# Optimization experiments

Measured on AMD Instinct MI355X. Metric: run time of the kernel, lower is better.

## Reference

```python
import jax, jax.numpy as jnp
import numpy as np

EMB_DIM = 1024
D_K = 64
B, S = 4, 4096

def setup_inputs() -> dict:
    key = jax.random.key(0)
    ks = jax.random.split(key, 8)
    inv = 1.0 / np.sqrt(EMB_DIM)
    return {
        "input1": jax.random.normal(ks[0], (B, S, EMB_DIM), dtype=jnp.float32),
        "input2": jax.random.normal(ks[1], (B, S, EMB_DIM), dtype=jnp.float32),
        "Wq": jax.random.uniform(ks[2], (EMB_DIM, D_K), jnp.float32, -inv, inv),
        "bq": jax.random.uniform(ks[3], (D_K,), jnp.float32, -inv, inv),
        "Wk": jax.random.uniform(ks[4], (EMB_DIM, D_K), jnp.float32, -inv, inv),
        "bk": jax.random.uniform(ks[5], (D_K,), jnp.float32, -inv, inv),
        "Wv": jax.random.uniform(ks[6], (EMB_DIM, D_K), jnp.float32, -inv, inv),
        "bv": jax.random.uniform(ks[7], (D_K,), jnp.float32, -inv, inv),
    }

def reference(input1, input2, Wq, bq, Wk, bk, Wv, bv):
    # queries from input2; keys/values from input1 (as in the torch forward)
    q = input2 @ Wq + bq            # [B, Sq, d_k]
    k = input1 @ Wk + bk            # [B, Sk, d_k]
    v = input1 @ Wv + bv            # [B, Sk, d_k]
    scale = 1.0 / jnp.sqrt(jnp.asarray(D_K, q.dtype))
    scores = jnp.einsum("bqd,bkd->bqk", q, k) * scale  # [B, Sq, Sk]
    attn = jax.nn.softmax(scores, axis=-1)
    return jnp.einsum("bqk,bkd->bqd", attn, v)          # [B, Sq, d_k]
```

## Files before the change

### kernel.cpp

```cpp
#include <hip/hip_runtime.h>
#include <hip/hip_bf16.h>

#define E 1024
#define DK 64
#define SEQ 4096
#define NB 4
#define KSCALE 0.18033688011112042f

typedef short bf16x8 __attribute__((ext_vector_type(8)));
typedef short bf16x4 __attribute__((ext_vector_type(4)));
typedef float f32x4 __attribute__((ext_vector_type(4)));

typedef const __attribute__((address_space(1))) unsigned int* gcp;
typedef __attribute__((address_space(3))) unsigned int* lcp;

__device__ inline unsigned short f2bf(float f) {
    unsigned int u = __float_as_uint(f);
    u += 0x7fff + ((u >> 16) & 1);
    return (unsigned short)(u >> 16);
}
__device__ inline unsigned int cvtpk(float a, float b) {
    union { __hip_bfloat162 h; unsigned int u; } x;
    x.h = __float22bfloat162_rn(make_float2(a, b));
    return x.u;
}
__device__ inline bf16x8 cvt8(f32x4 a, f32x4 b) {
    union { unsigned int u[4]; bf16x8 v; } x;
    x.u[0] = cvtpk(a[0], a[1]); x.u[1] = cvtpk(a[2], a[3]);
    x.u[2] = cvtpk(b[0], b[1]); x.u[3] = cvtpk(b[2], b[3]);
    return x.v;
}

__global__ __launch_bounds__(256) void wt_kernel(
    const float* __restrict__ Wq, const float* __restrict__ Wk, const float* __restrict__ Wv,
    unsigned short* __restrict__ wtq, unsigned short* __restrict__ wtk, unsigned short* __restrict__ wtv)
{
    const float* src; unsigned short* dst;
    if (blockIdx.y == 0)      { src = Wq; dst = wtq; }
    else if (blockIdx.y == 1) { src = Wk; dst = wtk; }
    else                      { src = Wv; dst = wtv; }
    const int tid = threadIdx.x;
    const int e0 = blockIdx.x * 64;
    __shared__ float Ws[64][65];
    #pragma unroll
    for (int i = 0; i < 4; ++i) {
        int flat = i * 256 + tid;
        int r = flat >> 4;
        int c4 = (flat & 15) << 2;
        float4 v = *reinterpret_cast<const float4*>(&src[(size_t)(e0 + r) * DK + c4]);
        Ws[c4 + 0][r] = v.x; Ws[c4 + 1][r] = v.y; Ws[c4 + 2][r] = v.z; Ws[c4 + 3][r] = v.w;
    }
    __syncthreads();
    #pragma unroll
    for (int i = 0; i < 4; ++i) {
        int flat = i * 256 + tid;
        int c = flat >> 4;
        int r4 = (flat & 15) << 2;
        ushort4 o;
        o.x = f2bf(Ws[c][r4 + 0]); o.y = f2bf(Ws[c][r4 + 1]);
        o.z = f2bf(Ws[c][r4 + 2]); o.w = f2bf(Ws[c][r4 + 3]);
        *reinterpret_cast<ushort4*>(&dst[(size_t)c * E + e0 + r4]) = o;
    }
}

__global__ __launch_bounds__(256, 4) void proj_kernel(
    const float* __restrict__ in_q, const float* __restrict__ in_kv,
    const unsigned short* __restrict__ wtq, const unsigned short* __restrict__ wtk,
    const unsigned short* __restrict__ wtv,
    const float* __restrict__ bq, const float* __restrict__ bk, const float* __restrict__ bv,
    unsigned short* __restrict__ Qw, unsigned short* __restrict__ Kw, unsigned short* __restrict__ Vtw)
{
    const int tid = threadIdx.x;
    const int w = tid >> 6, lane = tid & 63, quad = lane >> 4, l16 = lane & 15;
    const int row0 = blockIdx.x * 64;
    const bool isQ = (blockIdx.y == 0);
    const float* Arow = (isQ ? in_q : in_kv) + (size_t)(row0 + w * 16 + l16) * E;
    const unsigned short* w0 = isQ ? wtq : wtk;

    __shared__ unsigned short W0s[2][4096];
    __shared__ unsigned short W1s[2][4096];

    const int rl = lane >> 3, pp = lane & 7;

    #pragma unroll
    for (int i = 0; i < 2; ++i) {
        int g = w * 2 + i;
        int r = g * 8 + rl;
        int lc = pp ^ (r & 7);
        __builtin_amdgcn_global_load_lds((gcp)(const void*)(w0 + (size_t)r * E + lc * 8),
                                         (lcp)(void*)&W0s[0][g * 512], 16, 0, 0);
        if (!isQ)
            __builtin_amdgcn_global_load_lds((gcp)(const void*)(wtv + (size_t)r * E + lc * 8),
                                             (lcp)(void*)&W1s[0][g * 512], 16, 0, 0);
    }
    f32x4 a_cur[4];
    #pragma unroll
    for (int ks = 0; ks < 2; ++ks)
        #pragma unroll
        for (int j = 0; j < 2; ++j)
            a_cur[ks * 2 + j] = *reinterpret_cast<const f32x4*>(Arow + ks * 32 + quad * 8 + j * 4);
    __syncthreads();

    f32x4 acc0[4] = {};
    f32x4 acc1[4] = {};

    for (int kb = 0; kb < 16; ++kb) {
        const int cur = kb & 1, nxt = cur ^ 1;
        f32x4 a_nxt[4];
        if (kb < 15) {
            const int ko = (kb + 1) * 64;
            #pragma unroll
            for (int i = 0; i < 2; ++i) {
                int g = w * 2 + i;
                int r = g * 8 + rl;
                int lc = pp ^ (r & 7);
                __builtin_amdgcn_global_load_lds((gcp)(const void*)(w0 + (size_t)r * E + ko + lc * 8),
                                                 (lcp)(void*)&W0s[nxt][g * 512], 16, 0, 0);
                if (!isQ)
                    __builtin_amdgcn_global_load_lds((gcp)(const void*)(wtv + (size_t)r * E + ko + lc * 8),
                                                     (lcp)(void*)&W1s[nxt][g * 512], 16, 0, 0);
            }
            const float* an = Arow + ko;
            #pragma unroll
            for (int ks = 0; ks < 2; ++ks)
                #pragma unroll
                for (int j = 0; j < 2; ++j)
                    a_nxt[ks * 2 + j] = *reinterpret_cast<const f32x4*>(an + ks * 32 + quad * 8 + j * 4);
        }
        #pragma unroll
        for (int ks = 0; ks < 2; ++ks) {
            bf16x8 af = cvt8(a_cur[ks * 2], a_cur[ks * 2 + 1]);
            #pragma unroll
            for (int ct = 0; ct < 4; ++ct) {
                int brow = ct * 16 + l16;
                int pc = (ks * 4 + quad) ^ (brow & 7);
                bf16x8 b0 = *reinterpret_cast<const bf16x8*>(&W0s[cur][brow * 64 + pc * 8]);
                acc0[ct] = __builtin_amdgcn_mfma_f32_16x16x32_bf16(af, b0, acc0[ct], 0, 0, 0);
                if (!isQ) {
                    bf16x8 b1 = *reinterpret_cast<const bf16x8*>(&W1s[cur][brow * 64 + pc * 8]);
                    acc1[ct] = __builtin_amdgcn_mfma_f32_16x16x32_bf16(af, b1, acc1[ct], 0, 0, 0);
                }
            }
        }
        #pragma unroll
        for (int j = 0; j < 4; ++j) a_cur[j] = a_nxt[j];
        if (kb < 15) __syncthreads();
    }

    const int orow0 = row0 + w * 16 + quad * 4;
    #pragma unroll
    for (int ct = 0; ct < 4; ++ct) {
        int col = ct * 16 + l16;
        if (isQ) {
            float bias = bq[col];
            #pragma unroll
            for (int r = 0; r < 4; ++r)
                Qw[(size_t)(orow0 + r) * DK + col] = f2bf(acc0[ct][r] + bias);
        } else {
            float biask = bk[col], biasv = bv[col];
            #pragma unroll
            for (int r = 0; r < 4; ++r) {
                int grow = orow0 + r;
                Kw[(size_t)grow * DK + col] = f2bf((acc0[ct][r] + biask) * KSCALE);
                int bb = grow >> 12;
                int tok = grow & 4095;
                Vtw[((size_t)(bb * 64 + col)) * SEQ + tok] = f2bf(acc1[ct][r] + biasv);
            }
        }
    }
}

__global__ __launch_bounds__(512) void attn_kernel(
    const unsigned short* __restrict__ Qw, const unsigned short* __restrict__ Kw,
    const unsigned short* __restrict__ Vtw, float* __restrict__ Opart, float* __restrict__ Lpart)
{
    const int tid = threadIdx.x;
    const int w = tid >> 6, lane = tid & 63, quad = lane >> 4, l16 = lane & 15;
    const int s = w & 3, h = w >> 2;
    const int kh = blockIdx.x & 1;
    const int b  = (blockIdx.x >> 1) & 3;
    const int qt = blockIdx.x >> 3;

    __shared__ unsigned short Klds[2][8192];
    __shared__ unsigned short Vlds[2][8192];
    __shared__ float LDSf[8][2][16][68];
    __shared__ float LDSl[8][4][16];

    const unsigned short* Ksrc = Kw + ((size_t)b * SEQ + kh * 2048) * DK;
    const unsigned short* Vsrc = Vtw + (size_t)b * 64 * SEQ + kh * 2048;

    const int g0 = w * 2, g1 = w * 2 + 1;
    const int krow0 = g0 * 8 + (lane >> 3), krow1 = g1 * 8 + (lane >> 3);
    const int kcol = ((lane & 7) ^ (lane >> 3)) << 4;
    const int vrow0 = g0 * 4 + (lane >> 4), vrow1 = g1 * 4 + (lane >> 4);
    const int vcol0 = ((lane & 15) ^ (vrow0 & 7)) << 4;
    const int vcol1 = ((lane & 15) ^ (vrow1 & 7)) << 4;

    auto stage = [&](int t, int bb) {
        const char* kb = (const char*)Ksrc + (size_t)t * 16384;
        __builtin_amdgcn_global_load_lds((gcp)(const void*)(kb + krow0 * 128 + kcol),
                                         (lcp)(void*)((char*)Klds[bb] + g0 * 1024), 16, 0, 0);
        __builtin_amdgcn_global_load_lds((gcp)(const void*)(kb + krow1 * 128 + kcol),
                                         (lcp)(void*)((char*)Klds[bb] + g1 * 1024), 16, 0, 0);
        const char* vb = (const char*)Vsrc + t * 256;
        __builtin_amdgcn_global_load_lds((gcp)(const void*)(vb + (size_t)vrow0 * 8192 + vcol0),
                                         (lcp)(void*)((char*)Vlds[bb] + g0 * 1024), 16, 0, 0);
        __builtin_amdgcn_global_load_lds((gcp)(const void*)(vb + (size_t)vrow1 * 8192 + vcol1),
                                         (lcp)(void*)((char*)Vlds[bb] + g1 * 1024), 16, 0, 0);
    };

    stage(0, 0);

    bf16x8 qfb[2][4];
    #pragma unroll
    for (int ks = 0; ks < 2; ++ks)
        #pragma unroll
        for (int ct = 0; ct < 4; ++ct)
            qfb[ks][ct] = *reinterpret_cast<const bf16x8*>(
                &Qw[((size_t)(b * SEQ + qt * 128 + h * 64 + ct * 16 + l16)) * DK + ks * 32 + quad * 8]);

    const int kxor = (l16 & 7) << 4;
    unsigned kf_off[2][2];
    unsigned va_off[2][4];
    #pragma unroll
    for (int t2 = 0; t2 < 2; ++t2) {
        const int kr = s * 32 + t2 * 16 + l16;
        kf_off[t2][0] = (unsigned)(kr * 128 + ((quad * 16) ^ kxor));
        kf_off[t2][1] = (unsigned)(kr * 128 + ((64 + quad * 16) ^ kxor));
        #pragma unroll
        for (int ct = 0; ct < 4; ++ct)
            va_off[t2][ct] = (unsigned)((ct * 16 + l16) * 256 +
                                        ((s * 64 + t2 * 32 + quad * 8) ^ kxor));
    }

    __syncthreads();

    float lp[4] = {0.f, 0.f, 0.f, 0.f};
    f32x4 o[4][4] = {};

    #pragma unroll 1
    for (int i = 0; i < 16; ++i) {
        const int cur = i & 1;
        if (i < 15) stage(i + 1, cur ^ 1);

        #pragma unroll
        for (int t2 = 0; t2 < 2; ++t2) {
            bf16x8 kf0 = *reinterpret_cast<const bf16x8*>((const char*)Klds[cur] + kf_off[t2][0]);
            bf16x8 kf1 = *reinterpret_cast<const bf16x8*>((const char*)Klds[cur] + kf_off[t2][1]);
            bf16x4 va[4];
            #pragma unroll
            for (int ct = 0; ct < 4; ++ct)
                va[ct] = *reinterpret_cast<const bf16x4*>((const char*)Vlds[cur] + va_off[t2][ct]);

            f32x4 sacc[4] = {};
            #pragma unroll
            for (int ct = 0; ct < 4; ++ct) {
                sacc[ct] = __builtin_amdgcn_mfma_f32_16x16x32_bf16(kf0, qfb[0][ct], sacc[ct], 0, 0, 0);
                sacc[ct] = __builtin_amdgcn_mfma_f32_16x16x32_bf16(kf1, qfb[1][ct], sacc[ct], 0, 0, 0);
            }

            #pragma unroll
            for (int cq = 0; cq < 4; ++cq) {
                float p0 = __builtin_amdgcn_exp2f(sacc[cq][0]);
                float p1 = __builtin_amdgcn_exp2f(sacc[cq][1]);
                float p2 = __builtin_amdgcn_exp2f(sacc[cq][2]);
                float p3 = __builtin_amdgcn_exp2f(sacc[cq][3]);
                lp[cq] += (p0 + p1) + (p2 + p3);
                union { unsigned int u[2]; bf16x4 v; } pbu;
                pbu.u[0] = cvtpk(p0, p1);
                pbu.u[1] = cvtpk(p2, p3);
                bf16x4 pb = pbu.v;
                #pragma unroll
                for (int cd = 0; cd < 4; ++cd)
                    o[cd][cq] = __builtin_amdgcn_mfma_f32_16x16x16bf16_1k(va[cd], pb, o[cd][cq], 0, 0, 0);
            }
        }

        __syncthreads();
    }

    #pragma unroll
    for (int cq = 0; cq < 4; ++cq) {
        float t = lp[cq];
        t += __shfl_xor(t, 16, 64);
        t += __shfl_xor(t, 32, 64);
        lp[cq] = t;
    }
    if (lane < 16)
        #pragma unroll
        for (int cq = 0; cq < 4; ++cq)
            LDSl[w][cq][lane] = lp[cq];

    const int rowbase = b * SEQ + qt * 128;
    #pragma unroll
    for (int rr = 0; rr < 2; ++rr) {
        #pragma unroll
        for (int hh = 0; hh < 2; ++hh)
            #pragma unroll
            for (int cd = 0; cd < 4; ++cd)
                *reinterpret_cast<f32x4*>(&LDSf[w][hh][l16][cd * 16 + quad * 4]) = o[cd][rr * 2 + hh];
        __syncthreads();
        #pragma unroll
        for (int p = 0; p < 2; ++p) {
            const int item = tid + p * 512;
            const int h2 = item >> 9, rem = item & 511;
            const int j = rem >> 8, ql = (rem >> 4) & 15, d4 = (rem & 15) << 2;
            const int cq = rr * 2 + j;
            f32x4 acc = {};
            #pragma unroll
            for (int w2 = 0; w2 < 4; ++w2)
                acc += *reinterpret_cast<const f32x4*>(&LDSf[h2 * 4 + w2][j][ql][d4]);
            const int row = rowbase + h2 * 64 + cq * 16 + ql;
            *reinterpret_cast<f32x4*>(&Opart[((size_t)kh * (NB * SEQ) + row) * DK + d4]) = acc;
            if ((rem & 15) == 0) {
                float lq = 0.f;
                #pragma unroll
                for (int w2 = 0; w2 < 4; ++w2)
                    lq += LDSl[h2 * 4 + w2][cq][ql];
                Lpart[kh * (NB * SEQ) + row] = lq;
            }
        }
        __syncthreads();
    }
}

__global__ __launch_bounds__(256) void comb_kernel(
    const float* __restrict__ Op, const float* __restrict__ Lp, float* __restrict__ out)
{
    const int idx = blockIdx.x * 256 + threadIdx.x;
    #pragma unroll
    for (int it = 0; it < 4; ++it) {
        const int c = idx + it * 65536;
        const int row = c >> 4;
        const int d4 = (c & 15) << 2;
        f32x4 a = *reinterpret_cast<const f32x4*>(&Op[(size_t)row * DK + d4]);
        f32x4 b2 = *reinterpret_cast<const f32x4*>(&Op[(size_t)(NB * SEQ + row) * DK + d4]);
        float l = Lp[row] + Lp[NB * SEQ + row];
        f32x4 r = (a + b2) * (1.0f / l);
        *reinterpret_cast<f32x4*>(&out[(size_t)row * DK + d4]) = r;
    }
}

extern "C" void kernel_launch(void* const* d_in, const int* in_sizes, int n_in,
                              void* d_out, int out_size, void* d_ws, size_t ws_size,
                              hipStream_t stream) {
    const float* input1 = (const float*)d_in[0];
    const float* input2 = (const float*)d_in[1];
    const float* Wq = (const float*)d_in[2];
    const float* bq = (const float*)d_in[3];
    const float* Wk = (const float*)d_in[4];
    const float* bk = (const float*)d_in[5];
    const float* Wv = (const float*)d_in[6];
    const float* bv = (const float*)d_in[7];
    float* out = (float*)d_out;

    char* ws = (char*)d_ws;
    unsigned short* wtq = (unsigned short*)(ws + 0);
    unsigned short* wtk = (unsigned short*)(ws + 131072);
    unsigned short* wtv = (unsigned short*)(ws + 262144);
    unsigned short* Qw  = (unsigned short*)(ws + 393216);
    unsigned short* Kw  = (unsigned short*)(ws + 2490368);
    unsigned short* Vtw = (unsigned short*)(ws + 4587520);
    float* Opart = (float*)(ws + 6684672);
    float* Lpart = (float*)(ws + 15073280);

    wt_kernel<<<dim3(16, 3), 256, 0, stream>>>(Wq, Wk, Wv, wtq, wtk, wtv);
    proj_kernel<<<dim3(256, 2), 256, 0, stream>>>(input2, input1, wtq, wtk, wtv,
                                                  bq, bk, bv, Qw, Kw, Vtw);
    attn_kernel<<<dim3(256), 512, 0, stream>>>(Qw, Kw, Vtw, Opart, Lpart);
    comb_kernel<<<dim3(256), 256, 0, stream>>>(Opart, Lpart, out);
}
```

Baseline: 197.2 us.

## Split projection into separate Q/K/V blocks with smaller 32-row tiles

The projection kernel now launches 1536 blocks of 128 threads, each computing a single 32-row tile for one of Q, K or V. Before, K and V shared one block that read each input1 tile once, and those blocks did twice the work of the Q blocks. The split balances the load and raises parallelism across the GPU. In exchange, input1 is read twice from global memory (once for K, once for V), and each block reuses its weights over fewer rows.

```diff
diff --git a/kernel.cpp b/kernel.cpp
--- a/kernel.cpp
+++ b/kernel.cpp
@@ -63,7 +63,7 @@
     }
 }
 
-__global__ __launch_bounds__(256, 4) void proj_kernel(
+__global__ __launch_bounds__(128) void proj_kernel(
     const float* __restrict__ in_q, const float* __restrict__ in_kv,
     const unsigned short* __restrict__ wtq, const unsigned short* __restrict__ wtk,
     const unsigned short* __restrict__ wtv,
@@ -72,26 +72,24 @@
 {
     const int tid = threadIdx.x;
     const int w = tid >> 6, lane = tid & 63, quad = lane >> 4, l16 = lane & 15;
-    const int row0 = blockIdx.x * 64;
-    const bool isQ = (blockIdx.y == 0);
-    const float* Arow = (isQ ? in_q : in_kv) + (size_t)(row0 + w * 16 + l16) * E;
-    const unsigned short* w0 = isQ ? wtq : wtk;
+    const int bid = blockIdx.x;
+    const int tile = bid / 3, m = bid - tile * 3;
+    const int row0 = tile * 32;
+    const float* A0 = (m == 0) ? in_q : in_kv;
+    const unsigned short* w0 = (m == 0) ? wtq : (m == 1) ? wtk : wtv;
+    const float* Arow = A0 + (size_t)(row0 + w * 16 + l16) * E;
 
     __shared__ unsigned short W0s[2][4096];
-    __shared__ unsigned short W1s[2][4096];
 
     const int rl = lane >> 3, pp = lane & 7;
 
     #pragma unroll
-    for (int i = 0; i < 2; ++i) {
-        int g = w * 2 + i;
+    for (int i = 0; i < 4; ++i) {
+        int g = w * 4 + i;
         int r = g * 8 + rl;
         int lc = pp ^ (r & 7);
         __builtin_amdgcn_global_load_lds((gcp)(const void*)(w0 + (size_t)r * E + lc * 8),
                                          (lcp)(void*)&W0s[0][g * 512], 16, 0, 0);
-        if (!isQ)
-            __builtin_amdgcn_global_load_lds((gcp)(const void*)(wtv + (size_t)r * E + lc * 8),
-                                             (lcp)(void*)&W1s[0][g * 512], 16, 0, 0);
     }
     f32x4 a_cur[4];
     #pragma unroll
@@ -102,7 +100,6 @@
     __syncthreads();
 
     f32x4 acc0[4] = {};
-    f32x4 acc1[4] = {};
 
     for (int kb = 0; kb < 16; ++kb) {
         const int cur = kb & 1, nxt = cur ^ 1;
@@ -110,15 +107,12 @@
         if (kb < 15) {
             const int ko = (kb + 1) * 64;
             #pragma unroll
-            for (int i = 0; i < 2; ++i) {
-                int g = w * 2 + i;
+            for (int i = 0; i < 4; ++i) {
+                int g = w * 4 + i;
                 int r = g * 8 + rl;
                 int lc = pp ^ (r & 7);
                 __builtin_amdgcn_global_load_lds((gcp)(const void*)(w0 + (size_t)r * E + ko + lc * 8),
                                                  (lcp)(void*)&W0s[nxt][g * 512], 16, 0, 0);
-                if (!isQ)
-                    __builtin_amdgcn_global_load_lds((gcp)(const void*)(wtv + (size_t)r * E + ko + lc * 8),
-                                                     (lcp)(void*)&W1s[nxt][g * 512], 16, 0, 0);
             }
             const float* an = Arow + ko;
             #pragma unroll
@@ -136,10 +130,6 @@
                 int pc = (ks * 4 + quad) ^ (brow & 7);
                 bf16x8 b0 = *reinterpret_cast<const bf16x8*>(&W0s[cur][brow * 64 + pc * 8]);
                 acc0[ct] = __builtin_amdgcn_mfma_f32_16x16x32_bf16(af, b0, acc0[ct], 0, 0, 0);
-                if (!isQ) {
-                    bf16x8 b1 = *reinterpret_cast<const bf16x8*>(&W1s[cur][brow * 64 + pc * 8]);
-                    acc1[ct] = __builtin_amdgcn_mfma_f32_16x16x32_bf16(af, b1, acc1[ct], 0, 0, 0);
-                }
             }
         }
         #pragma unroll
@@ -151,20 +141,24 @@
     #pragma unroll
     for (int ct = 0; ct < 4; ++ct) {
         int col = ct * 16 + l16;
-        if (isQ) {
+        if (m == 0) {
             float bias = bq[col];
             #pragma unroll
             for (int r = 0; r < 4; ++r)
                 Qw[(size_t)(orow0 + r) * DK + col] = f2bf(acc0[ct][r] + bias);
+        } else if (m == 1) {
+            float biask = bk[col];
+            #pragma unroll
+            for (int r = 0; r < 4; ++r)
+                Kw[(size_t)(orow0 + r) * DK + col] = f2bf((acc0[ct][r] + biask) * KSCALE);
         } else {
-            float biask = bk[col], biasv = bv[col];
+            float biasv = bv[col];
             #pragma unroll
             for (int r = 0; r < 4; ++r) {
                 int grow = orow0 + r;
-                Kw[(size_t)grow * DK + col] = f2bf((acc0[ct][r] + biask) * KSCALE);
                 int bb = grow >> 12;
                 int tok = grow & 4095;
-                Vtw[((size_t)(bb * 64 + col)) * SEQ + tok] = f2bf(acc1[ct][r] + biasv);
+                Vtw[((size_t)(bb * 64 + col)) * SEQ + tok] = f2bf(acc0[ct][r] + biasv);
             }
         }
     }
@@ -365,8 +359,8 @@
     float* Lpart = (float*)(ws + 15073280);
 
     wt_kernel<<<dim3(16, 3), 256, 0, stream>>>(Wq, Wk, Wv, wtq, wtk, wtv);
-    proj_kernel<<<dim3(256, 2), 256, 0, stream>>>(input2, input1, wtq, wtk, wtv,
-                                                  bq, bk, bv, Qw, Kw, Vtw);
+    proj_kernel<<<dim3(1536), 128, 0, stream>>>(input2, input1, wtq, wtk, wtv,
+                                                bq, bk, bv, Qw, Kw, Vtw);
     attn_kernel<<<dim3(256), 512, 0, stream>>>(Qw, Kw, Vtw, Opart, Lpart);
     comb_kernel<<<dim3(256), 256, 0, stream>>>(Opart, Lpart, out);
 }
```

Measured after the change: 211.2 us. +7.1%, slower.
